# Optimization experiments

Measured on AMD Instinct MI355X. Metric: run time of the kernel, lower is better.

## Reference

```python
import jax, jax.numpy as jnp
import numpy as np

V, P, C, M, P_ORIG, T = 81920, 131072, 512, 1024, 163840, 262144


def setup_inputs() -> dict:
    key = jax.random.key(0)
    ks = jax.random.split(key, 6)
    adapter_feat = jax.random.normal(ks[0], (V, C), dtype=jnp.float32)
    ce = jax.random.normal(ks[1], (M, C), dtype=jnp.float32)
    # caption embeddings arrive pre-normalized in the original pipeline
    caption_embed = ce / jnp.clip(jnp.linalg.norm(ce, axis=-1, keepdims=True), 1e-12)
    logit_scale = jnp.full((1,), np.log(1.0 / 0.07), dtype=jnp.float32)  # learnable param init
    v2p_map = jax.random.randint(ks[2], (P,), 0, V, dtype=jnp.int32)
    origin_idx = jax.random.randint(ks[3], (P,), 0, P_ORIG, dtype=jnp.int32)
    caption_to_point_mapping = jax.random.randint(ks[4], (T,), 0, P_ORIG, dtype=jnp.int32)
    caption_seg_idx = jnp.sort(jax.random.randint(ks[5], (T,), 0, M, dtype=jnp.int32))
    return {
        "adapter_feat": adapter_feat,
        "caption_embed": caption_embed,
        "logit_scale": logit_scale,
        "v2p_map": v2p_map,
        "origin_idx": origin_idx,
        "caption_to_point_mapping": caption_to_point_mapping,
        "caption_seg_idx": caption_seg_idx,
        "n_origin_points": P_ORIG,
    }


def reference(adapter_feat, caption_embed, logit_scale, v2p_map, origin_idx,
              caption_to_point_mapping, caption_seg_idx, n_origin_points):
    n_pts = v2p_map.shape[0]
    n_captions = caption_embed.shape[0]

    # gather voxel features to points, L2-normalize (feat_norm=True)
    feats = adapter_feat[v2p_map]                                       # [P, C]
    feats = feats / jnp.clip(jnp.linalg.norm(feats, axis=-1, keepdims=True), 1e-12)

    # per-point log-softmax caption scores
    logits = (feats @ caption_embed.T) * jnp.exp(logit_scale[0])        # [P, M]
    scores = jax.nn.log_softmax(logits, axis=-1)                        # [P, M]

    # origin-point -> current-point mapping; -1 where origin point was dropped
    ptom = jnp.full((n_origin_points,), -1, dtype=jnp.int32)
    ptom = ptom.at[origin_idx].set(jnp.arange(n_pts, dtype=jnp.int32))

    gidx = ptom[caption_to_point_mapping]                               # [T]
    invalid = (gidx < 0).astype(scores.dtype)                           # [T]
    # torch negative advanced indexing wraps; replicate faithfully
    safe = jnp.where(gidx < 0, gidx + n_pts, gidx)
    gathered = scores[safe]                                             # [T, M]

    # scatter-sum scores and counts per caption segment
    pooled = jax.ops.segment_sum(gathered, caption_seg_idx, num_segments=n_captions)
    cnt = jax.ops.segment_sum(jnp.ones_like(invalid), caption_seg_idx, num_segments=n_captions)
    ninv = jax.ops.segment_sum(invalid, caption_seg_idx, num_segments=n_captions)
    real_n_points = cnt - ninv                                          # [N]

    denom = jnp.where(real_n_points > 0,
                      1.0 / jnp.where(real_n_points > 0, real_n_points, 1.0), 0.0)
    pooled = pooled * denom[:, None]                                    # [N, M]
    if_has_pts = real_n_points > 0
    return pooled, real_n_points, if_has_pts
```

## Files before the change

### kernel.cpp

```cpp
#include <hip/hip_runtime.h>

#define P_PTS 131072
#define CDIM  512
#define MCAP  1024
#define TLEN  262144
#define PORIG 163840

typedef unsigned short u16;
typedef unsigned char  u8;
typedef __attribute__((ext_vector_type(8))) short short8;
typedef __attribute__((ext_vector_type(4))) float f32x4;
typedef __attribute__((ext_vector_type(8))) int int8v;
typedef __attribute__((ext_vector_type(4))) int int4v;

__device__ __forceinline__ u16 f2bf(float f) {
    unsigned u = __float_as_uint(f);
    unsigned r = (u + 0x7FFFu + ((u >> 16) & 1u)) >> 16;
    return (u16)r;
}
__device__ __forceinline__ float d_e4m3(unsigned x) {
    float f = __uint_as_float((x & 0x7Fu) << 20) * 0x1p120f;
    return __uint_as_float(__float_as_uint(f) | ((x & 0x80u) << 24));
}
__device__ __forceinline__ void ld16(const void* g, void* l) {
    __builtin_amdgcn_global_load_lds(
        (const __attribute__((address_space(1))) void*)g,
        (__attribute__((address_space(3))) void*)l, 16, 0, 0);
}

__global__ __launch_bounds__(256) void gather_prep(
    const float* __restrict__ adapter, const int* __restrict__ v2p,
    const float* __restrict__ cap, const int* __restrict__ oidx,
    u8* __restrict__ feats8, u16* __restrict__ capb, u8* __restrict__ Bswz,
    int* __restrict__ ptom, float* __restrict__ lse_sum) {
    int b = blockIdx.x, tid = threadIdx.x;
    if (b < 32768) {
        int p = b * 4 + (tid >> 6);
        int lane = tid & 63;
        int vrow = v2p[p];
        const float4* src = (const float4*)(adapter + (size_t)vrow * CDIM);
        float4 x0 = src[lane * 2];
        float4 x1 = src[lane * 2 + 1];
        float ss = x0.x*x0.x + x0.y*x0.y + x0.z*x0.z + x0.w*x0.w
                 + x1.x*x1.x + x1.y*x1.y + x1.z*x1.z + x1.w*x1.w;
        #pragma unroll
        for (int off = 32; off >= 1; off >>= 1) ss += __shfl_xor(ss, off, 64);
        float inv = 1.0f / fmaxf(sqrtf(ss), 1e-12f);
        int lo = __builtin_amdgcn_cvt_pk_fp8_f32(x0.x*inv, x0.y*inv, 0, false);
        lo = __builtin_amdgcn_cvt_pk_fp8_f32(x0.z*inv, x0.w*inv, lo, true);
        int hi = __builtin_amdgcn_cvt_pk_fp8_f32(x1.x*inv, x1.y*inv, 0, false);
        hi = __builtin_amdgcn_cvt_pk_fp8_f32(x1.z*inv, x1.w*inv, hi, true);
        uint2 w; w.x = (unsigned)lo; w.y = (unsigned)hi;
        *(uint2*)(feats8 + (size_t)p * CDIM + lane * 8) = w;
    } else if (b < 33280) {
        int t = (b - 32768) * 256 + tid;
        int i = t * 4;
        float4 v = *(const float4*)(cap + i);
        u16* o = capb + i;
        o[0] = f2bf(v.x); o[1] = f2bf(v.y); o[2] = f2bf(v.z); o[3] = f2bf(v.w);
        atomicMax(&ptom[oidx[t]], t);
    } else if (b < 33792) {
        int j = (b - 33280) * 256 + tid;
        lse_sum[j] = 0.0f;
    } else {
        int g2 = (b - 33792) * 256 + tid;
        int c    = g2 & 1;
        int lane = (g2 >> 1) & 63;
        int j    = (g2 >> 7) & 3;
        int kk   = (g2 >> 9) & 3;
        int wn   = (g2 >> 11) & 1;
        int c0   = g2 >> 12;
        int col  = c0 * 128 + wn * 64 + j * 16 + (lane & 15);
        int kb   = kk * 128 + (lane >> 4) * 32 + c * 16;
        const float* s = cap + (size_t)col * CDIM + kb;
        unsigned w4[4];
        #pragma unroll
        for (int u = 0; u < 4; ++u) {
            int p = __builtin_amdgcn_cvt_pk_fp8_f32(s[u*4+0], s[u*4+1], 0, false);
            p = __builtin_amdgcn_cvt_pk_fp8_f32(s[u*4+2], s[u*4+3], p, true);
            w4[u] = (unsigned)p;
        }
        *(uint4*)(Bswz + (size_t)g2 * 16) = *(uint4*)w4;
    }
}

__global__ __launch_bounds__(256) void lse_gemm(
    const u8* __restrict__ feats8, const u8* __restrict__ Bswz,
    const float* __restrict__ lsc, float* __restrict__ lse_sum,
    const int* __restrict__ ctpm, const int* __restrict__ ptom,
    unsigned* __restrict__ rows) {
    if (blockIdx.x >= 8192) {
        int t = (blockIdx.x - 8192) * 256 + threadIdx.x;
        int g = ptom[ctpm[t]];
        rows[t] = (g < 0) ? ((unsigned)(g + P_PTS) | 0x80000000u) : (unsigned)g;
        return;
    }
    __shared__ __align__(16) u8 As[16384];
    const int tid  = threadIdx.x;
    const int wave = tid >> 6;
    const int lane = tid & 63;
    const unsigned id = blockIdx.x;
    const int c0   = (int)((id >> 3) & 7u);
    const int col0 = c0 * 128;
    const int row0 = (int)((id & 7u) + 8u * (id >> 6)) * 128;
    const int wm = (wave >> 1) * 64;
    const int wn1 = (wave & 1);
    const float sf = __expf(lsc[0]);

    f32x4 acc[4][4] = {};

    const int srow = tid >> 3;
    const int kc   = (tid & 7) ^ (srow & 7);
    const u8* gA = feats8 + (size_t)(row0 + srow) * CDIM + kc * 16;
    u8* lA = As + wave * 1024;

    const int m = lane & 15;
    const int q = lane >> 4;
    const u8* rA1 = As + (size_t)((wm + m) * 8 + ((2*q)   ^ (m & 7))) * 16;
    const u8* rA2 = As + (size_t)((wm + m) * 8 + ((2*q+1) ^ (m & 7))) * 16;
    const u8* bw = Bswz + (size_t)(c0 * 2 + wn1) * 16 * 2048 + lane * 32;

    #pragma unroll
    for (int k0 = 0; k0 < CDIM; k0 += 128) {
        const int kk = k0 >> 7;
        int8v bv[4];
        #pragma unroll
        for (int j = 0; j < 4; ++j) {
            int4v lo = *(const int4v*)(bw + (kk * 4 + j) * 2048);
            int4v hi = *(const int4v*)(bw + (kk * 4 + j) * 2048 + 16);
            bv[j][0]=lo[0]; bv[j][1]=lo[1]; bv[j][2]=lo[2]; bv[j][3]=lo[3];
            bv[j][4]=hi[0]; bv[j][5]=hi[1]; bv[j][6]=hi[2]; bv[j][7]=hi[3];
        }
        __syncthreads();
        #pragma unroll
        for (int c = 0; c < 4; ++c)
            ld16(gA + (size_t)c * 32 * CDIM + k0, lA + c * 4096);
        __syncthreads();
        int8v af[4];
        #pragma unroll
        for (int i = 0; i < 4; ++i) {
            int4v lo = *(const int4v*)(rA1 + i * 2048);
            int4v hi = *(const int4v*)(rA2 + i * 2048);
            af[i][0]=lo[0]; af[i][1]=lo[1]; af[i][2]=lo[2]; af[i][3]=lo[3];
            af[i][4]=hi[0]; af[i][5]=hi[1]; af[i][6]=hi[2]; af[i][7]=hi[3];
        }
        #pragma unroll
        for (int i = 0; i < 4; ++i)
            #pragma unroll
            for (int j = 0; j < 4; ++j)
                acc[i][j] = __builtin_amdgcn_mfma_scale_f32_16x16x128_f8f6f4(
                    af[i], bv[j], acc[i][j], 0, 0, 0, 127, 0, 127);
    }

    #pragma unroll
    for (int i = 0; i < 4; ++i) {
        float s4[4] = {0.f, 0.f, 0.f, 0.f};
        #pragma unroll
        for (int j = 0; j < 4; ++j)
            #pragma unroll
            for (int r = 0; r < 4; ++r)
                s4[r] += __expf(acc[i][j][r] * sf - sf);
        #pragma unroll
        for (int off = 8; off >= 1; off >>= 1)
            #pragma unroll
            for (int r = 0; r < 4; ++r)
                s4[r] += __shfl_xor(s4[r], off, 64);
        if (m == 0) {
            int rbase = row0 + wm + i * 16 + q * 4;
            #pragma unroll
            for (int r = 0; r < 4; ++r)
                atomicAdd(&lse_sum[rbase + r], s4[r]);
        }
    }
}

__device__ __forceinline__ int lower_bound(const int* __restrict__ a, int n, int key) {
    int lo = 0, hi = n;
    while (lo < hi) { int mid = (lo + hi) >> 1; if (a[mid] < key) lo = mid + 1; else hi = mid; }
    return lo;
}

__global__ __launch_bounds__(1024) void seg_reduce(
    const u8* __restrict__ feats8, const float* __restrict__ lse_sum,
    const unsigned* __restrict__ rows, const int* __restrict__ seg,
    const float* __restrict__ lsc,
    u16* __restrict__ Fb, float* __restrict__ Lout, float* __restrict__ realn) {
    int s = blockIdx.x;
    int tid = threadIdx.x, wave = tid >> 6, lane = tid & 63;
    int start = lower_bound(seg, TLEN, s);
    int end   = lower_bound(seg, TLEN, s + 1);
    float a[8] = {0,0,0,0,0,0,0,0};
    float Lacc = 0.f; int inv = 0;
    int r = start + wave;
    for (; r + 16 < end; r += 32) {
        unsigned p0 = rows[r], p1 = rows[r + 16];
        int r0 = (int)(p0 & 0x7FFFFFFFu), r1 = (int)(p1 & 0x7FFFFFFFu);
        uint2 v0 = *(const uint2*)(feats8 + (size_t)r0 * CDIM + lane * 8);
        uint2 v1 = *(const uint2*)(feats8 + (size_t)r1 * CDIM + lane * 8);
        if (lane == 0) {
            inv += (int)(p0 >> 31) + (int)(p1 >> 31);
            Lacc += __logf(lse_sum[r0]) + __logf(lse_sum[r1]);
        }
        a[0] += d_e4m3(v0.x);       a[1] += d_e4m3(v0.x >> 8);
        a[2] += d_e4m3(v0.x >> 16); a[3] += d_e4m3(v0.x >> 24);
        a[4] += d_e4m3(v0.y);       a[5] += d_e4m3(v0.y >> 8);
        a[6] += d_e4m3(v0.y >> 16); a[7] += d_e4m3(v0.y >> 24);
        a[0] += d_e4m3(v1.x);       a[1] += d_e4m3(v1.x >> 8);
        a[2] += d_e4m3(v1.x >> 16); a[3] += d_e4m3(v1.x >> 24);
        a[4] += d_e4m3(v1.y);       a[5] += d_e4m3(v1.y >> 8);
        a[6] += d_e4m3(v1.y >> 16); a[7] += d_e4m3(v1.y >> 24);
    }
    if (r < end) {
        unsigned p0 = rows[r];
        int r0 = (int)(p0 & 0x7FFFFFFFu);
        uint2 v0 = *(const uint2*)(feats8 + (size_t)r0 * CDIM + lane * 8);
        if (lane == 0) { inv += (int)(p0 >> 31); Lacc += __logf(lse_sum[r0]); }
        a[0] += d_e4m3(v0.x);       a[1] += d_e4m3(v0.x >> 8);
        a[2] += d_e4m3(v0.x >> 16); a[3] += d_e4m3(v0.x >> 24);
        a[4] += d_e4m3(v0.y);       a[5] += d_e4m3(v0.y >> 8);
        a[6] += d_e4m3(v0.y >> 16); a[7] += d_e4m3(v0.y >> 24);
    }
    __shared__ float pF[16][512];
    __shared__ float pL[16];
    __shared__ int   pI[16];
    #pragma unroll
    for (int u = 0; u < 8; ++u) pF[wave][lane * 8 + u] = a[u];
    if (lane == 0) { pL[wave] = Lacc; pI[wave] = inv; }
    __syncthreads();
    if (tid < 512) {
        float f = 0.f;
        #pragma unroll
        for (int w = 0; w < 16; ++w) f += pF[w][tid];
        Fb[(size_t)s * CDIM + tid] = f2bf(f);
    }
    if (tid == 0) {
        float cnt = (float)(end - start);
        float Ls = 0.f; int ninv = 0;
        #pragma unroll
        for (int w = 0; w < 16; ++w) { Ls += pL[w]; ninv += pI[w]; }
        realn[s] = cnt - (float)ninv;
        Lout[s] = Ls + __expf(lsc[0]) * cnt;
    }
}

__global__ __launch_bounds__(256) void pooled_gemm(
    const u16* __restrict__ Fb, const u16* __restrict__ capb,
    const float* __restrict__ Lout, const float* __restrict__ realn,
    const float* __restrict__ lsc, float* __restrict__ out) {
    __shared__ __align__(16) u16 As[64 * 32];
    __shared__ __align__(16) u16 Bs[64 * 32];
    const int tid  = threadIdx.x;
    const int wave = tid >> 6;
    const int lane = tid & 63;
    const int col0 = blockIdx.x * 64;
    const int row0 = blockIdx.y * 64;
    const int wm = (wave >> 1) * 32;
    const int wn = (wave & 1) * 32;
    const float sf = __expf(lsc[0]);
    f32x4 acc[2][2] = {};
    const int srow = tid >> 2;
    const int scol = (tid & 3) * 8;
    const u16* gA0 = Fb   + (size_t)(row0 + srow) * CDIM + scol;
    const u16* gB0 = capb + (size_t)(col0 + srow) * CDIM + scol;
    u16* lA0 = As + wave * 512;
    u16* lB0 = Bs + wave * 512;
    const int mrow = lane & 15;
    const int quad = lane >> 4;
    const u16* rA = As + (wm + mrow) * 32 + quad * 8;
    const u16* rB = Bs + (wn + mrow) * 32 + quad * 8;
    #pragma unroll 4
    for (int k0 = 0; k0 < CDIM; k0 += 32) {
        __syncthreads();
        ld16(gA0 + k0, lA0);
        ld16(gB0 + k0, lB0);
        __syncthreads();
        short8 af[2], bfr[2];
        #pragma unroll
        for (int i = 0; i < 2; ++i) af[i]  = *(const short8*)(rA + i * 512);
        #pragma unroll
        for (int j = 0; j < 2; ++j) bfr[j] = *(const short8*)(rB + j * 512);
        #pragma unroll
        for (int i = 0; i < 2; ++i)
            #pragma unroll
            for (int j = 0; j < 2; ++j)
                acc[i][j] = __builtin_amdgcn_mfma_f32_16x16x32_bf16(
                    af[i], bfr[j], acc[i][j], 0, 0, 0);
    }
    #pragma unroll
    for (int i = 0; i < 2; ++i) {
        #pragma unroll
        for (int r = 0; r < 4; ++r) {
            int s = row0 + wm + i * 16 + quad * 4 + r;
            float rn = realn[s];
            float dn = rn > 0.f ? 1.0f / rn : 0.0f;
            float L = Lout[s];
            #pragma unroll
            for (int j = 0; j < 2; ++j) {
                int mc = col0 + wn + j * 16 + mrow;
                out[(size_t)s * MCAP + mc] = (sf * acc[i][j][r] - L) * dn;
            }
        }
    }
    if (col0 == 0 && tid < 64) {
        int s = row0 + tid;
        float rv = realn[s];
        out[MCAP * MCAP + s] = rv;
        out[MCAP * MCAP + MCAP + s] = (rv > 0.f) ? 1.0f : 0.0f;
    }
}

extern "C" void kernel_launch(void* const* d_in, const int* in_sizes, int n_in,
                              void* d_out, int out_size, void* d_ws, size_t ws_size,
                              hipStream_t stream) {
    const float* adapter = (const float*)d_in[0];
    const float* cap     = (const float*)d_in[1];
    const float* lsc     = (const float*)d_in[2];
    const int*   v2p     = (const int*)d_in[3];
    const int*   oidx    = (const int*)d_in[4];
    const int*   ctpm    = (const int*)d_in[5];
    const int*   seg     = (const int*)d_in[6];
    float* out = (float*)d_out;

    char* ws = (char*)d_ws;
    u8*       feats8  = (u8*)(ws);
    u16*      capb    = (u16*)(ws + 67108864);
    u8*       Bswz    = (u8*)(ws + 68157440);
    float*    lse_sum = (float*)(ws + 68681728);
    int*      ptom    = (int*)(ws + 69206016);
    unsigned* rows    = (unsigned*)(ws + 69861376);
    u16*      Fb      = (u16*)(ws + 70909952);
    float*    Lout    = (float*)(ws + 71958528);
    float*    realn   = (float*)(ws + 71962624);

    hipMemsetAsync(ptom, 0xFF, (size_t)PORIG * 4, stream);

    gather_prep<<<33920, 256, 0, stream>>>(adapter, v2p, cap, oidx,
                                           feats8, capb, Bswz, ptom, lse_sum);
    lse_gemm<<<8192 + TLEN / 256, 256, 0, stream>>>(feats8, Bswz, lsc, lse_sum,
                                                    ctpm, ptom, rows);
    seg_reduce<<<MCAP, 1024, 0, stream>>>(feats8, lse_sum, rows, seg, lsc, Fb, Lout, realn);
    pooled_gemm<<<dim3(MCAP / 64, MCAP / 64), 256, 0, stream>>>(Fb, capb, Lout, realn, lsc, out);
}
```

Before: 401.9 us.

## Load GEMM operand fragments directly from global memory, dropping LDS staging

Both the fp8 logit GEMM and the bf16 pooled GEMM stop staging A (and B in the pooled GEMM) tiles through shared memory with async global-to-LDS copies. Each wave now reads its MFMA fragments straight from global memory. This removes the two __syncthreads per k-step and the LDS traffic, and lets the compiler fully unroll and schedule the loads. In exchange, data shared between waves is fetched redundantly through the cache, and each row is read in strided 16–32 byte pieces, which may hurt coalescing.

Result: slower. 465.0 us (+15.7%).

```diff
diff --git a/kernel.cpp b/kernel.cpp
--- a/kernel.cpp
+++ b/kernel.cpp
@@ -21,11 +21,6 @@
 __device__ __forceinline__ float d_e4m3(unsigned x) {
     float f = __uint_as_float((x & 0x7Fu) << 20) * 0x1p120f;
     return __uint_as_float(__float_as_uint(f) | ((x & 0x80u) << 24));
-}
-__device__ __forceinline__ void ld16(const void* g, void* l) {
-    __builtin_amdgcn_global_load_lds(
-        (const __attribute__((address_space(1))) void*)g,
-        (__attribute__((address_space(3))) void*)l, 16, 0, 0);
 }
 
 __global__ __launch_bounds__(256) void gather_prep(
@@ -95,13 +90,11 @@
         rows[t] = (g < 0) ? ((unsigned)(g + P_PTS) | 0x80000000u) : (unsigned)g;
         return;
     }
-    __shared__ __align__(16) u8 As[16384];
     const int tid  = threadIdx.x;
     const int wave = tid >> 6;
     const int lane = tid & 63;
     const unsigned id = blockIdx.x;
     const int c0   = (int)((id >> 3) & 7u);
-    const int col0 = c0 * 128;
     const int row0 = (int)((id & 7u) + 8u * (id >> 6)) * 128;
     const int wm = (wave >> 1) * 64;
     const int wn1 = (wave & 1);
@@ -109,15 +102,9 @@
 
     f32x4 acc[4][4] = {};
 
-    const int srow = tid >> 3;
-    const int kc   = (tid & 7) ^ (srow & 7);
-    const u8* gA = feats8 + (size_t)(row0 + srow) * CDIM + kc * 16;
-    u8* lA = As + wave * 1024;
-
     const int m = lane & 15;
     const int q = lane >> 4;
-    const u8* rA1 = As + (size_t)((wm + m) * 8 + ((2*q)   ^ (m & 7))) * 16;
-    const u8* rA2 = As + (size_t)((wm + m) * 8 + ((2*q+1) ^ (m & 7))) * 16;
+    const u8* gA = feats8 + (size_t)(row0 + wm + m) * CDIM + q * 32;
     const u8* bw = Bswz + (size_t)(c0 * 2 + wn1) * 16 * 2048 + lane * 32;
 
     #pragma unroll
@@ -131,16 +118,12 @@
             bv[j][0]=lo[0]; bv[j][1]=lo[1]; bv[j][2]=lo[2]; bv[j][3]=lo[3];
             bv[j][4]=hi[0]; bv[j][5]=hi[1]; bv[j][6]=hi[2]; bv[j][7]=hi[3];
         }
-        __syncthreads();
-        #pragma unroll
-        for (int c = 0; c < 4; ++c)
-            ld16(gA + (size_t)c * 32 * CDIM + k0, lA + c * 4096);
-        __syncthreads();
         int8v af[4];
         #pragma unroll
         for (int i = 0; i < 4; ++i) {
-            int4v lo = *(const int4v*)(rA1 + i * 2048);
-            int4v hi = *(const int4v*)(rA2 + i * 2048);
+            const u8* a = gA + (size_t)(i * 16) * CDIM + k0;
+            int4v lo = *(const int4v*)(a);
+            int4v hi = *(const int4v*)(a + 16);
             af[i][0]=lo[0]; af[i][1]=lo[1]; af[i][2]=lo[2]; af[i][3]=lo[3];
             af[i][4]=hi[0]; af[i][5]=hi[1]; af[i][6]=hi[2]; af[i][7]=hi[3];
         }
@@ -247,8 +230,6 @@
     const u16* __restrict__ Fb, const u16* __restrict__ capb,
     const float* __restrict__ Lout, const float* __restrict__ realn,
     const float* __restrict__ lsc, float* __restrict__ out) {
-    __shared__ __align__(16) u16 As[64 * 32];
-    __shared__ __align__(16) u16 Bs[64 * 32];
     const int tid  = threadIdx.x;
     const int wave = tid >> 6;
     const int lane = tid & 63;
@@ -258,27 +239,19 @@
     const int wn = (wave & 1) * 32;
     const float sf = __expf(lsc[0]);
     f32x4 acc[2][2] = {};
-    const int srow = tid >> 2;
-    const int scol = (tid & 3) * 8;
-    const u16* gA0 = Fb   + (size_t)(row0 + srow) * CDIM + scol;
-    const u16* gB0 = capb + (size_t)(col0 + srow) * CDIM + scol;
-    u16* lA0 = As + wave * 512;
-    u16* lB0 = Bs + wave * 512;
     const int mrow = lane & 15;
     const int quad = lane >> 4;
-    const u16* rA = As + (wm + mrow) * 32 + quad * 8;
-    const u16* rB = Bs + (wn + mrow) * 32 + quad * 8;
-    #pragma unroll 4
+    const u16* gA = Fb   + (size_t)(row0 + wm + mrow) * CDIM + quad * 8;
+    const u16* gB = capb + (size_t)(col0 + wn + mrow) * CDIM + quad * 8;
+    #pragma unroll
     for (int k0 = 0; k0 < CDIM; k0 += 32) {
-        __syncthreads();
-        ld16(gA0 + k0, lA0);
-        ld16(gB0 + k0, lB0);
-        __syncthreads();
         short8 af[2], bfr[2];
         #pragma unroll
-        for (int i = 0; i < 2; ++i) af[i]  = *(const short8*)(rA + i * 512);
-        #pragma unroll
-        for (int j = 0; j < 2; ++j) bfr[j] = *(const short8*)(rB + j * 512);
+        for (int i = 0; i < 2; ++i)
+            af[i]  = *(const short8*)(gA + (size_t)(i * 16) * CDIM + k0);
+        #pragma unroll
+        for (int j = 0; j < 2; ++j)
+            bfr[j] = *(const short8*)(gB + (size_t)(j * 16) * CDIM + k0);
         #pragma unroll
         for (int i = 0; i < 2; ++i)
             #pragma unroll
```
